# Performance work log

Measured on AMD Instinct MI355X. Metric: run time of the kernel, lower is better.

The kernel has to match this reference:

```python
import jax, jax.numpy as jnp
import numpy as np

THRESHOLD = 1.0
DECAY = 0.95
T, B, N_IN = 16, 512, 3072
S1, S2, S3 = 256, 256, 128
E = 8


def _lif_step(v, h):
    # LIF membrane update: decay, integrate, threshold-spike, soft reset.
    v = v * DECAY + h
    spk = (v >= THRESHOLD).astype(v.dtype)
    return spk, v - spk * THRESHOLD


def setup_inputs() -> dict:
    key = jax.random.key(0)
    k_seq, k1, k2, k3 = jax.random.split(key, 4)
    # Binary spike train input (rate-coded), shape (T, B, N_in)
    spike_seq = (jax.random.uniform(k_seq, (T, B, N_IN)) < 0.5).astype(jnp.float32)
    # Expert weights: nn.Linear weight layout is (out, in); init N(0, 0.05)
    W1 = 0.05 * jax.random.normal(k1, (E, S1, N_IN), dtype=jnp.float32)
    W2 = 0.05 * jax.random.normal(k2, (E, S2, S1), dtype=jnp.float32)
    W3 = 0.05 * jax.random.normal(k3, (E, S3, S2), dtype=jnp.float32)
    # Uniform gates 1/num_experts (requires_grad=False buffers in the original)
    g = jnp.full((E,), 1.0 / E, dtype=jnp.float32)
    return {"spike_seq": spike_seq, "W1": W1, "W2": W2, "W3": W3,
            "g1": g, "g2": g, "g3": g}


def reference(spike_seq, W1, W2, W3, g1, g2, g3):
    t, b = spike_seq.shape[0], spike_seq.shape[1]
    x = spike_seq.reshape(t, b, -1)
    e = W1.shape[0]
    dt = x.dtype
    v1 = jnp.zeros((e, b, W1.shape[1]), dt)
    v2 = jnp.zeros((e, b, W2.shape[1]), dt)
    v3 = jnp.zeros((e, b, W3.shape[1]), dt)

    def step(carry, xt):
        v1, v2, v3 = carry
        # stage 1: batched per-expert GEMM + LIF + gated combine
        h1 = jnp.einsum('bi,eoi->ebo', xt, W1)
        spk1, v1 = _lif_step(v1, h1)
        c1 = jnp.einsum('e,ebo->bo', g1, spk1)
        # stage 2
        h2 = jnp.einsum('bi,eoi->ebo', c1, W2)
        spk2, v2 = _lif_step(v2, h2)
        c2 = jnp.einsum('e,ebo->bo', g2, spk2)
        # stage 3
        h3 = jnp.einsum('bi,eoi->ebo', c2, W3)
        spk3, v3 = _lif_step(v3, h3)
        c3 = jnp.einsum('e,ebo->bo', g3, spk3)
        return (v1, v2, v3), (c1, c2, c3)

    _, (s1, s2, s3) = jax.lax.scan(step, (v1, v2, v3), x)
    # time-averaged combined outputs per stage
    return s1.mean(axis=0), s2.mean(axis=0), s3.mean(axis=0)
```

## Files before the change

### kernel.cpp

```cpp
#include <hip/hip_runtime.h>
#include <hip/hip_bf16.h>
#include <cmath>

#define T_STEPS 16
#define BATCH   512
#define N_IN    3072
#define S1      256
#define S2      256
#define S3      128
#define NEXP    8
#define M_ROWS  (T_STEPS * BATCH)
#define MT_ALL  (M_ROWS / 32)

typedef int v4i  __attribute__((ext_vector_type(4)));
typedef int v16i __attribute__((ext_vector_type(16)));
typedef unsigned long long u64;
typedef unsigned int uint32;

__global__ __launch_bounds__(256) void pack_x_bits(
    const float* __restrict__ x, u64* __restrict__ bitsT)
{
    int gid = blockIdx.x * 256 + threadIdx.x;
    float v = x[gid];
    u64 m = __ballot(v >= 0.5f);
    if ((threadIdx.x & 63) == 0) {
        int tb = gid / N_IN;
        int k  = gid - tb * N_IN;
        int t  = tb >> 9;
        int b  = tb & 511;
        bitsT[(size_t)(k >> 6) * M_ROWS + (b * 16 + t)] = m;
    }
}

template<int S, int K>
__global__ __launch_bounds__(256) void digitize_w_frag(
    const float* __restrict__ W, char* __restrict__ Bf)
{
    constexpr int LOGS = (S == 256) ? 8 : 7;
    int t = blockIdx.x * 256 + threadIdx.x;
    int lane16 = t & 63;
    int o  = (t >> 6) & (S - 1);
    int kb = t >> (6 + LOGS);
    int r  = lane16 & 31;
    int qd = lane16 >> 5;
    int e    = r >> 2;
    int limb = r & 3;
    int k0 = kb * 32 + qd * 16;

    const float4* Wp = (const float4*)(W + ((size_t)e * S + o) * K + k0);
    char out[16];
    #pragma unroll
    for (int f4 = 0; f4 < 4; ++f4) {
        float4 w = Wp[f4];
        float ws[4] = {w.x, w.y, w.z, w.w};
        #pragma unroll
        for (int c = 0; c < 4; ++c) {
            long long q = llrint((double)ws[c] * 4294967296.0);
            int d = 0;
            #pragma unroll
            for (int l = 0; l < 4; ++l) {
                int dl = (int)((q + 128) & 255) - 128;
                q = (q - dl) >> 8;
                if (l == limb) d = dl;
            }
            out[f4 * 4 + c] = (char)d;
        }
    }
    *(v4i*)(Bf + (size_t)t * 16) = *(v4i*)out;
}

template<int K, int S, int SHIFT, bool ABITS, bool WRITEC, int NBLK>
__global__ __launch_bounds__(256, 3) void fused_stage(
    const void* __restrict__ Ap, const char* __restrict__ Bf,
    const float* __restrict__ g, char* __restrict__ Cf,
    float* __restrict__ Mean)
{
    constexpr int KI = K / 64;
    constexpr int NT = S;
    constexpr int NS = NBLK / 8;
    __shared__ double hs[256][16];

    const int tid  = threadIdx.x;
    const int lane = tid & 63;
    const int w    = tid >> 6;
    const int col  = lane & 31;
    const int qd   = lane >> 5;
    const int wm   = w * 64;

    const int id   = blockIdx.x;
    const int nblk = (id & 7) * NS + ((id >> 3) % NS);
    const int mblk = id / NBLK;
    const int m0   = mblk * 256;

    const int nt0 = nblk * 2;
    const char* Bbase = Bf + ((size_t)nt0 * 64 + lane) * 16;

    v16i acc[2][2];
    #pragma unroll
    for (int i = 0; i < 2; ++i)
        #pragma unroll
        for (int j = 0; j < 2; ++j)
            #pragma unroll
            for (int r = 0; r < 16; ++r) acc[i][j][r] = 0;

    auto loadB = [&](int kb, int jj) -> v4i {
        return *(const v4i*)(Bbase + (size_t)kb * (NT * 1024) + jj * 1024);
    };

    v4i Bb[3][4];

    if constexpr (ABITS) {
        const u64* AT = (const u64*)Ap + (m0 + wm + col);
        const int sh16 = qd * 16;
        auto unpack16 = [&](uint32 dw) -> v4i {
            uint32 w16 = dw >> sh16;
            v4i d;
            #pragma unroll
            for (int c = 0; c < 4; ++c)
                d[c] = (int)((((w16 >> (4 * c)) & 0xFu) * 0x00204081u) & 0x01010101u);
            return d;
        };
        u64 a0b[3], a1b[3];
        #pragma unroll
        for (int s = 0; s < 2; ++s) {
            #pragma unroll
            for (int ks = 0; ks < 2; ++ks)
                #pragma unroll
                for (int jj = 0; jj < 2; ++jj)
                    Bb[s][ks * 2 + jj] = loadB(s * 2 + ks, jj);
            a0b[s] = AT[(size_t)s * M_ROWS];
            a1b[s] = AT[(size_t)s * M_ROWS + 32];
        }
        auto body = [&](int it, int cur, int pf) {
            const int itp = (it + 2 < KI) ? it + 2 : KI - 1;
            #pragma unroll
            for (int ks = 0; ks < 2; ++ks)
                #pragma unroll
                for (int jj = 0; jj < 2; ++jj)
                    Bb[pf][ks * 2 + jj] = loadB(itp * 2 + ks, jj);
            a0b[pf] = AT[(size_t)itp * M_ROWS];
            a1b[pf] = AT[(size_t)itp * M_ROWS + 32];
            #pragma unroll
            for (int ks = 0; ks < 2; ++ks) {
                uint32 dw0 = ks ? (uint32)(a0b[cur] >> 32) : (uint32)a0b[cur];
                uint32 dw1 = ks ? (uint32)(a1b[cur] >> 32) : (uint32)a1b[cur];
                v4i af0 = unpack16(dw0);
                v4i af1 = unpack16(dw1);
                acc[0][0] = __builtin_amdgcn_mfma_i32_32x32x32_i8(af0, Bb[cur][ks*2+0], acc[0][0], 0,0,0);
                acc[0][1] = __builtin_amdgcn_mfma_i32_32x32x32_i8(af0, Bb[cur][ks*2+1], acc[0][1], 0,0,0);
                acc[1][0] = __builtin_amdgcn_mfma_i32_32x32x32_i8(af1, Bb[cur][ks*2+0], acc[1][0], 0,0,0);
                acc[1][1] = __builtin_amdgcn_mfma_i32_32x32x32_i8(af1, Bb[cur][ks*2+1], acc[1][1], 0,0,0);
            }
        };
        static_assert(KI % 3 == 0, "stage-1 KI divisible by 3");
        for (int itb = 0; itb < KI; itb += 3) {
            body(itb + 0, 0, 2);
            body(itb + 1, 1, 0);
            body(itb + 2, 2, 1);
        }
    } else {
        const int mt0 = (m0 + wm) >> 5;
        const char* Abase = (const char*)Ap + ((size_t)mt0 * 64 + lane) * 16;
        auto loadA = [&](int kb, int ii) -> v4i {
            return *(const v4i*)(Abase + (size_t)kb * (MT_ALL * 1024) + ii * 1024);
        };
        v4i Ab[3][4];
        #pragma unroll
        for (int s = 0; s < 2; ++s) {
            #pragma unroll
            for (int ks = 0; ks < 2; ++ks) {
                Ab[s][ks * 2 + 0] = loadA(s * 2 + ks, 0);
                Ab[s][ks * 2 + 1] = loadA(s * 2 + ks, 1);
                #pragma unroll
                for (int jj = 0; jj < 2; ++jj)
                    Bb[s][ks * 2 + jj] = loadB(s * 2 + ks, jj);
            }
        }
        auto body = [&](int it, int cur, int pf) {
            const int itp = (it + 2 < KI) ? it + 2 : KI - 1;
            #pragma unroll
            for (int ks = 0; ks < 2; ++ks) {
                Ab[pf][ks * 2 + 0] = loadA(itp * 2 + ks, 0);
                Ab[pf][ks * 2 + 1] = loadA(itp * 2 + ks, 1);
                #pragma unroll
                for (int jj = 0; jj < 2; ++jj)
                    Bb[pf][ks * 2 + jj] = loadB(itp * 2 + ks, jj);
            }
            #pragma unroll
            for (int ks = 0; ks < 2; ++ks) {
                acc[0][0] = __builtin_amdgcn_mfma_i32_32x32x32_i8(Ab[cur][ks*2+0], Bb[cur][ks*2+0], acc[0][0], 0,0,0);
                acc[0][1] = __builtin_amdgcn_mfma_i32_32x32x32_i8(Ab[cur][ks*2+0], Bb[cur][ks*2+1], acc[0][1], 0,0,0);
                acc[1][0] = __builtin_amdgcn_mfma_i32_32x32x32_i8(Ab[cur][ks*2+1], Bb[cur][ks*2+0], acc[1][0], 0,0,0);
                acc[1][1] = __builtin_amdgcn_mfma_i32_32x32x32_i8(Ab[cur][ks*2+1], Bb[cur][ks*2+1], acc[1][1], 0,0,0);
            }
        };
        static_assert(KI == 4, "stages 2/3 have KI=4");
        body(0, 0, 2);
        body(1, 1, 0);
        body(2, 2, 1);
        body(3, 0, 2);
    }

    const double sbase = 1.0 / (double)(1ll << SHIFT);
    const int limb = col & 3;
    const double lscale = (double)(1 << (8 * limb)) * sbase;
    #pragma unroll
    for (int j = 0; j < 2; ++j) {
        const int oe = j * 8 + (col >> 2);
        #pragma unroll
        for (int i = 0; i < 2; ++i) {
            #pragma unroll
            for (int reg = 0; reg < 16; ++reg) {
                double d = (double)acc[i][j][reg] * lscale;
                d += __shfl_xor(d, 1);
                d += __shfl_xor(d, 2);
                if ((col & 3) == 0) {
                    int m = wm + i * 32 + (reg & 3) + 8 * (reg >> 2) + 4 * qd;
                    hs[m][oe] = d;
                }
            }
        }
    }
    __syncthreads();

    const int b_loc  = tid >> 4;
    const int o_loc  = (tid >> 3) & 1;
    const int e      = tid & 7;
    const int oe     = o_loc * 8 + e;
    const float ge   = g[e];
    const int bg = mblk * 16 + b_loc;
    const int og = nblk * 2 + o_loc;

    const int kb_a   = og >> 5;
    const int qd_a   = (og >> 4) & 1;
    const int byte_a = og & 15;

    double v = 0.0;
    float gacc = 0.0f;
    #pragma unroll
    for (int t = 0; t < T_STEPS; ++t) {
        double h  = hs[b_loc * 16 + t][oe];
        double vv = v * 0.95 + h;
        int spk = (vv >= 1.0) ? 1 : 0;
        v = vv - (double)spk;
        float gs = ge * (float)spk;
        gs += __shfl_xor(gs, 1);
        gs += __shfl_xor(gs, 2);
        gs += __shfl_xor(gs, 4);
        gacc += gs;
        if (WRITEC) {
            int cnt = spk;
            cnt += __shfl_xor(cnt, 1);
            cnt += __shfl_xor(cnt, 2);
            cnt += __shfl_xor(cnt, 4);
            if (e == 0) {
                int mp = bg * 16 + t;
                int lane_a = (mp & 31) + 32 * qd_a;
                Cf[(((size_t)kb_a * MT_ALL + (mp >> 5)) * 64 + lane_a) * 16 + byte_a]
                    = (char)cnt;
            }
        }
    }
    if (e == 0) Mean[(size_t)bg * S + og] = gacc * 0.0625f;
}

extern "C" void kernel_launch(void* const* d_in, const int* in_sizes, int n_in,
                              void* d_out, int out_size, void* d_ws, size_t ws_size,
                              hipStream_t stream) {
    const float* x  = (const float*)d_in[0];
    const float* W1 = (const float*)d_in[1];
    const float* W2 = (const float*)d_in[2];
    const float* W3 = (const float*)d_in[3];
    const float* g1 = (const float*)d_in[4];
    const float* g2 = (const float*)d_in[5];
    const float* g3 = (const float*)d_in[6];
    float* out = (float*)d_out;

    char* ws = (char*)d_ws;
    u64*  AbitsT = (u64*)ws;
    char* B1f    = ws + 3145728ull;
    char* B2f    = ws + 28311552ull;
    char* B3f    = ws + 30408704ull;
    char* c1f    = ws + 31457280ull;
    char* c2f    = ws + 33554432ull;

    dim3 blk(256);

    pack_x_bits<<<(M_ROWS * N_IN) / 256, blk, 0, stream>>>(x, AbitsT);
    digitize_w_frag<S1, N_IN><<<(2 * S1 * N_IN) / 256, blk, 0, stream>>>(W1, B1f);
    digitize_w_frag<S2, S1><<<(2 * S2 * S1) / 256, blk, 0, stream>>>(W2, B2f);
    digitize_w_frag<S3, S2><<<(2 * S3 * S2) / 256, blk, 0, stream>>>(W3, B3f);

    fused_stage<N_IN, S1, 32, true,  true,  128><<<32 * 128, blk, 0, stream>>>(
        AbitsT, B1f, g1, c1f, out);
    fused_stage<S1,   S2, 35, false, true,  128><<<32 * 128, blk, 0, stream>>>(
        c1f, B2f, g2, c2f, out + BATCH * S1);
    fused_stage<S2,   S3, 35, false, false, 64><<<32 * 64, blk, 0, stream>>>(
        c2f, B3f, g3, nullptr, out + BATCH * (S1 + S2));
}
```

Before: 542.8 us.

## Widen GEMM N-tile to four fragments and merge prep kernels into one launch

Each fused_stage block now covers four output N-tiles (32 expert-output columns) instead of two. This halves the block count and doubles reuse of the A fragments and unpacked spike bits per load. The prefetch pipeline drops from triple to double buffering, launch bounds go from 3 to 2 waves per SIMD, and LDS doubles to hold the wider tile. The four preprocessing kernels (bit packing and three weight digitizations) are merged into one launch to cut launch overhead. In exchange there is more register pressure, lower occupancy and less prefetch distance.

```diff
diff --git a/kernel.cpp b/kernel.cpp
--- a/kernel.cpp
+++ b/kernel.cpp
@@ -17,30 +17,22 @@
 typedef unsigned long long u64;
 typedef unsigned int uint32;
 
-__global__ __launch_bounds__(256) void pack_x_bits(
-    const float* __restrict__ x, u64* __restrict__ bitsT)
+__device__ __forceinline__ v4i unpack16_bits(uint32 w16)
 {
-    int gid = blockIdx.x * 256 + threadIdx.x;
-    float v = x[gid];
-    u64 m = __ballot(v >= 0.5f);
-    if ((threadIdx.x & 63) == 0) {
-        int tb = gid / N_IN;
-        int k  = gid - tb * N_IN;
-        int t  = tb >> 9;
-        int b  = tb & 511;
-        bitsT[(size_t)(k >> 6) * M_ROWS + (b * 16 + t)] = m;
-    }
+    v4i d;
+    #pragma unroll
+    for (int c = 0; c < 4; ++c)
+        d[c] = (int)((((w16 >> (4 * c)) & 0xFu) * 0x00204081u) & 0x01010101u);
+    return d;
 }
 
 template<int S, int K>
-__global__ __launch_bounds__(256) void digitize_w_frag(
-    const float* __restrict__ W, char* __restrict__ Bf)
+__device__ __forceinline__ void digitize_chunk(
+    const float* __restrict__ W, char* __restrict__ Bf, int t)
 {
-    constexpr int LOGS = (S == 256) ? 8 : 7;
-    int t = blockIdx.x * 256 + threadIdx.x;
     int lane16 = t & 63;
     int o  = (t >> 6) & (S - 1);
-    int kb = t >> (6 + LOGS);
+    int kb = t >> ((S == 256) ? 14 : 13);
     int r  = lane16 & 31;
     int qd = lane16 >> 5;
     int e    = r >> 2;
@@ -69,16 +61,45 @@
     *(v4i*)(Bf + (size_t)t * 16) = *(v4i*)out;
 }
 
+__global__ __launch_bounds__(256) void prep(
+    const float* __restrict__ x,  const float* __restrict__ W1,
+    const float* __restrict__ W2, const float* __restrict__ W3,
+    u64* __restrict__ bitsT, char* __restrict__ B1f,
+    char* __restrict__ B2f,  char* __restrict__ B3f)
+{
+    const int bid = blockIdx.x;
+    const int tid = threadIdx.x;
+    if (bid < 98304) {
+        int gid = bid * 256 + tid;
+        float v = x[gid];
+        u64 m = __ballot(v >= 0.5f);
+        if ((tid & 63) == 0) {
+            int tb = gid / N_IN;
+            int k  = gid - tb * N_IN;
+            int t  = tb >> 9;
+            int b  = tb & 511;
+            bitsT[(size_t)(k >> 6) * M_ROWS + (b * 16 + t)] = m;
+        }
+    } else if (bid < 98304 + 6144) {
+        digitize_chunk<S1, N_IN>(W1, B1f, (bid - 98304) * 256 + tid);
+    } else if (bid < 98304 + 6144 + 512) {
+        digitize_chunk<S2, S1>(W2, B2f, (bid - 98304 - 6144) * 256 + tid);
+    } else {
+        digitize_chunk<S3, S2>(W3, B3f, (bid - 98304 - 6656) * 256 + tid);
+    }
+}
+
 template<int K, int S, int SHIFT, bool ABITS, bool WRITEC, int NBLK>
-__global__ __launch_bounds__(256, 3) void fused_stage(
+__global__ __launch_bounds__(256, 2) void fused_stage(
     const void* __restrict__ Ap, const char* __restrict__ Bf,
     const float* __restrict__ g, char* __restrict__ Cf,
     float* __restrict__ Mean)
 {
     constexpr int KI = K / 64;
+    static_assert(KI % 2 == 0, "KI must be even");
     constexpr int NT = S;
     constexpr int NS = NBLK / 8;
-    __shared__ double hs[256][16];
+    __shared__ double hs[256][32];
 
     const int tid  = threadIdx.x;
     const int lane = tid & 63;
@@ -92,14 +113,14 @@
     const int mblk = id / NBLK;
     const int m0   = mblk * 256;
 
-    const int nt0 = nblk * 2;
+    const int nt0 = nblk * 4;
     const char* Bbase = Bf + ((size_t)nt0 * 64 + lane) * 16;
 
-    v16i acc[2][2];
+    v16i acc[2][4];
     #pragma unroll
     for (int i = 0; i < 2; ++i)
         #pragma unroll
-        for (int j = 0; j < 2; ++j)
+        for (int j = 0; j < 4; ++j)
             #pragma unroll
             for (int r = 0; r < 16; ++r) acc[i][j][r] = 0;
 
@@ -107,56 +128,46 @@
         return *(const v4i*)(Bbase + (size_t)kb * (NT * 1024) + jj * 1024);
     };
 
-    v4i Bb[3][4];
+    v4i Bb[2][8];
 
     if constexpr (ABITS) {
         const u64* AT = (const u64*)Ap + (m0 + wm + col);
         const int sh16 = qd * 16;
-        auto unpack16 = [&](uint32 dw) -> v4i {
-            uint32 w16 = dw >> sh16;
-            v4i d;
-            #pragma unroll
-            for (int c = 0; c < 4; ++c)
-                d[c] = (int)((((w16 >> (4 * c)) & 0xFu) * 0x00204081u) & 0x01010101u);
-            return d;
-        };
-        u64 a0b[3], a1b[3];
-        #pragma unroll
-        for (int s = 0; s < 2; ++s) {
+        u64 a0b[2], a1b[2];
+
+        a0b[0] = AT[0];
+        a1b[0] = AT[32];
+        #pragma unroll
+        for (int ks = 0; ks < 2; ++ks)
+            #pragma unroll
+            for (int jj = 0; jj < 4; ++jj)
+                Bb[0][ks * 4 + jj] = loadB(ks, jj);
+
+        auto body = [&](int it, int cur, int pf) {
+            const int itp = (it + 1 < KI) ? it + 1 : KI - 1;
+            a0b[pf] = AT[(size_t)itp * M_ROWS];
+            a1b[pf] = AT[(size_t)itp * M_ROWS + 32];
             #pragma unroll
             for (int ks = 0; ks < 2; ++ks)
                 #pragma unroll
-                for (int jj = 0; jj < 2; ++jj)
-                    Bb[s][ks * 2 + jj] = loadB(s * 2 + ks, jj);
-            a0b[s] = AT[(size_t)s * M_ROWS];
-            a1b[s] = AT[(size_t)s * M_ROWS + 32];
-        }
-        auto body = [&](int it, int cur, int pf) {
-            const int itp = (it + 2 < KI) ? it + 2 : KI - 1;
-            #pragma unroll
-            for (int ks = 0; ks < 2; ++ks)
-                #pragma unroll
-                for (int jj = 0; jj < 2; ++jj)
-                    Bb[pf][ks * 2 + jj] = loadB(itp * 2 + ks, jj);
-            a0b[pf] = AT[(size_t)itp * M_ROWS];
-            a1b[pf] = AT[(size_t)itp * M_ROWS + 32];
+                for (int jj = 0; jj < 4; ++jj)
+                    Bb[pf][ks * 4 + jj] = loadB(itp * 2 + ks, jj);
             #pragma unroll
             for (int ks = 0; ks < 2; ++ks) {
                 uint32 dw0 = ks ? (uint32)(a0b[cur] >> 32) : (uint32)a0b[cur];
                 uint32 dw1 = ks ? (uint32)(a1b[cur] >> 32) : (uint32)a1b[cur];
-                v4i af0 = unpack16(dw0);
-                v4i af1 = unpack16(dw1);
-                acc[0][0] = __builtin_amdgcn_mfma_i32_32x32x32_i8(af0, Bb[cur][ks*2+0], acc[0][0], 0,0,0);
-                acc[0][1] = __builtin_amdgcn_mfma_i32_32x32x32_i8(af0, Bb[cur][ks*2+1], acc[0][1], 0,0,0);
-                acc[1][0] = __builtin_amdgcn_mfma_i32_32x32x32_i8(af1, Bb[cur][ks*2+0], acc[1][0], 0,0,0);
-                acc[1][1] = __builtin_amdgcn_mfma_i32_32x32x32_i8(af1, Bb[cur][ks*2+1], acc[1][1], 0,0,0);
+                v4i af0 = unpack16_bits(dw0 >> sh16);
+                v4i af1 = unpack16_bits(dw1 >> sh16);
+                #pragma unroll
+                for (int jj = 0; jj < 4; ++jj) {
+                    acc[0][jj] = __builtin_amdgcn_mfma_i32_32x32x32_i8(af0, Bb[cur][ks*4+jj], acc[0][jj], 0,0,0);
+                    acc[1][jj] = __builtin_amdgcn_mfma_i32_32x32x32_i8(af1, Bb[cur][ks*4+jj], acc[1][jj], 0,0,0);
+                }
             }
         };
-        static_assert(KI % 3 == 0, "stage-1 KI divisible by 3");
-        for (int itb = 0; itb < KI; itb += 3) {
-            body(itb + 0, 0, 2);
+        for (int itb = 0; itb < KI; itb += 2) {
+            body(itb + 0, 0, 1);
             body(itb + 1, 1, 0);
-            body(itb + 2, 2, 1);
         }
     } else {
         const int mt0 = (m0 + wm) >> 5;
@@ -164,48 +175,46 @@
         auto loadA = [&](int kb, int ii) -> v4i {
             return *(const v4i*)(Abase + (size_t)kb * (MT_ALL * 1024) + ii * 1024);
         };
-        v4i Ab[3][4];
-        #pragma unroll
-        for (int s = 0; s < 2; ++s) {
-            #pragma unroll
-            for (int ks = 0; ks < 2; ++ks) {
-                Ab[s][ks * 2 + 0] = loadA(s * 2 + ks, 0);
-                Ab[s][ks * 2 + 1] = loadA(s * 2 + ks, 1);
-                #pragma unroll
-                for (int jj = 0; jj < 2; ++jj)
-                    Bb[s][ks * 2 + jj] = loadB(s * 2 + ks, jj);
-            }
-        }
+        v4i Ab[2][4];
+
+        #pragma unroll
+        for (int ks = 0; ks < 2; ++ks) {
+            Ab[0][ks * 2 + 0] = loadA(ks, 0);
+            Ab[0][ks * 2 + 1] = loadA(ks, 1);
+            #pragma unroll
+            for (int jj = 0; jj < 4; ++jj)
+                Bb[0][ks * 4 + jj] = loadB(ks, jj);
+        }
+
         auto body = [&](int it, int cur, int pf) {
-            const int itp = (it + 2 < KI) ? it + 2 : KI - 1;
+            const int itp = (it + 1 < KI) ? it + 1 : KI - 1;
             #pragma unroll
             for (int ks = 0; ks < 2; ++ks) {
                 Ab[pf][ks * 2 + 0] = loadA(itp * 2 + ks, 0);
                 Ab[pf][ks * 2 + 1] = loadA(itp * 2 + ks, 1);
                 #pragma unroll
-                for (int jj = 0; jj < 2; ++jj)
-                    Bb[pf][ks * 2 + jj] = loadB(itp * 2 + ks, jj);
-            }
-            #pragma unroll
-            for (int ks = 0; ks < 2; ++ks) {
-                acc[0][0] = __builtin_amdgcn_mfma_i32_32x32x32_i8(Ab[cur][ks*2+0], Bb[cur][ks*2+0], acc[0][0], 0,0,0);
-                acc[0][1] = __builtin_amdgcn_mfma_i32_32x32x32_i8(Ab[cur][ks*2+0], Bb[cur][ks*2+1], acc[0][1], 0,0,0);
-                acc[1][0] = __builtin_amdgcn_mfma_i32_32x32x32_i8(Ab[cur][ks*2+1], Bb[cur][ks*2+0], acc[1][0], 0,0,0);
-                acc[1][1] = __builtin_amdgcn_mfma_i32_32x32x32_i8(Ab[cur][ks*2+1], Bb[cur][ks*2+1], acc[1][1], 0,0,0);
-            }
+                for (int jj = 0; jj < 4; ++jj)
+                    Bb[pf][ks * 4 + jj] = loadB(itp * 2 + ks, jj);
+            }
+            #pragma unroll
+            for (int ks = 0; ks < 2; ++ks)
+                #pragma unroll
+                for (int jj = 0; jj < 4; ++jj) {
+                    acc[0][jj] = __builtin_amdgcn_mfma_i32_32x32x32_i8(Ab[cur][ks*2+0], Bb[cur][ks*4+jj], acc[0][jj], 0,0,0);
+                    acc[1][jj] = __builtin_amdgcn_mfma_i32_32x32x32_i8(Ab[cur][ks*2+1], Bb[cur][ks*4+jj], acc[1][jj], 0,0,0);
+                }
         };
-        static_assert(KI == 4, "stages 2/3 have KI=4");
-        body(0, 0, 2);
-        body(1, 1, 0);
-        body(2, 2, 1);
-        body(3, 0, 2);
+        for (int itb = 0; itb < KI; itb += 2) {
+            body(itb + 0, 0, 1);
+            body(itb + 1, 1, 0);
+        }
     }
 
     const double sbase = 1.0 / (double)(1ll << SHIFT);
     const int limb = col & 3;
     const double lscale = (double)(1 << (8 * limb)) * sbase;
     #pragma unroll
-    for (int j = 0; j < 2; ++j) {
+    for (int j = 0; j < 4; ++j) {
         const int oe = j * 8 + (col >> 2);
         #pragma unroll
         for (int i = 0; i < 2; ++i) {
@@ -224,44 +233,49 @@
     __syncthreads();
 
     const int b_loc  = tid >> 4;
-    const int o_loc  = (tid >> 3) & 1;
+    const int ol2    = (tid >> 3) & 1;
     const int e      = tid & 7;
-    const int oe     = o_loc * 8 + e;
     const float ge   = g[e];
     const int bg = mblk * 16 + b_loc;
-    const int og = nblk * 2 + o_loc;
-
-    const int kb_a   = og >> 5;
-    const int qd_a   = (og >> 4) & 1;
-    const int byte_a = og & 15;
-
-    double v = 0.0;
-    float gacc = 0.0f;
-    #pragma unroll
-    for (int t = 0; t < T_STEPS; ++t) {
-        double h  = hs[b_loc * 16 + t][oe];
-        double vv = v * 0.95 + h;
-        int spk = (vv >= 1.0) ? 1 : 0;
-        v = vv - (double)spk;
-        float gs = ge * (float)spk;
-        gs += __shfl_xor(gs, 1);
-        gs += __shfl_xor(gs, 2);
-        gs += __shfl_xor(gs, 4);
-        gacc += gs;
-        if (WRITEC) {
-            int cnt = spk;
-            cnt += __shfl_xor(cnt, 1);
-            cnt += __shfl_xor(cnt, 2);
-            cnt += __shfl_xor(cnt, 4);
-            if (e == 0) {
-                int mp = bg * 16 + t;
-                int lane_a = (mp & 31) + 32 * qd_a;
-                Cf[(((size_t)kb_a * MT_ALL + (mp >> 5)) * 64 + lane_a) * 16 + byte_a]
-                    = (char)cnt;
-            }
-        }
-    }
-    if (e == 0) Mean[(size_t)bg * S + og] = gacc * 0.0625f;
+
+    #pragma unroll
+    for (int p = 0; p < 2; ++p) {
+        const int o_loc = p * 2 + ol2;
+        const int oe    = o_loc * 8 + e;
+        const int og    = nblk * 4 + o_loc;
+
+        const int kb_a   = og >> 5;
+        const int qd_a   = (og >> 4) & 1;
+        const int byte_a = og & 15;
+
+        double v = 0.0;
+        float gacc = 0.0f;
+        #pragma unroll
+        for (int t = 0; t < T_STEPS; ++t) {
+            double h  = hs[b_loc * 16 + t][oe];
+            double vv = v * 0.95 + h;
+            int spk = (vv >= 1.0) ? 1 : 0;
+            v = vv - (double)spk;
+            float gs = ge * (float)spk;
+            gs += __shfl_xor(gs, 1);
+            gs += __shfl_xor(gs, 2);
+            gs += __shfl_xor(gs, 4);
+            gacc += gs;
+            if (WRITEC) {
+                int cnt = spk;
+                cnt += __shfl_xor(cnt, 1);
+                cnt += __shfl_xor(cnt, 2);
+                cnt += __shfl_xor(cnt, 4);
+                if (e == 0) {
+                    int mp = bg * 16 + t;
+                    int lane_a = (mp & 31) + 32 * qd_a;
+                    Cf[(((size_t)kb_a * MT_ALL + (mp >> 5)) * 64 + lane_a) * 16 + byte_a]
+                        = (char)cnt;
+                }
+            }
+        }
+        if (e == 0) Mean[(size_t)bg * S + og] = gacc * 0.0625f;
+    }
 }
 
 extern "C" void kernel_launch(void* const* d_in, const int* in_sizes, int n_in,
@@ -286,15 +300,13 @@
 
     dim3 blk(256);
 
-    pack_x_bits<<<(M_ROWS * N_IN) / 256, blk, 0, stream>>>(x, AbitsT);
-    digitize_w_frag<S1, N_IN><<<(2 * S1 * N_IN) / 256, blk, 0, stream>>>(W1, B1f);
-    digitize_w_frag<S2, S1><<<(2 * S2 * S1) / 256, blk, 0, stream>>>(W2, B2f);
-    digitize_w_frag<S3, S2><<<(2 * S3 * S2) / 256, blk, 0, stream>>>(W3, B3f);
-
-    fused_stage<N_IN, S1, 32, true,  true,  128><<<32 * 128, blk, 0, stream>>>(
+    prep<<<98304 + 6144 + 512 + 256, blk, 0, stream>>>(
+        x, W1, W2, W3, AbitsT, B1f, B2f, B3f);
+
+    fused_stage<N_IN, S1, 32, true,  true,  64><<<32 * 64, blk, 0, stream>>>(
         AbitsT, B1f, g1, c1f, out);
-    fused_stage<S1,   S2, 35, false, true,  128><<<32 * 128, blk, 0, stream>>>(
+    fused_stage<S1,   S2, 35, false, true,  64><<<32 * 64, blk, 0, stream>>>(
         c1f, B2f, g2, c2f, out + BATCH * S1);
-    fused_stage<S2,   S3, 35, false, false, 64><<<32 * 64, blk, 0, stream>>>(
+    fused_stage<S2,   S3, 35, false, false, 32><<<32 * 32, blk, 0, stream>>>(
         c2f, B3f, g3, nullptr, out + BATCH * (S1 + S2));
 }
```

New measurement: 597.2 us. +10.0%, slower.
